# Optimization experiments

Hardware: AMD Instinct MI355X
Metric: run time of the kernel (lower is better)

## Reference

```python
import jax, jax.numpy as jnp
import numpy as np
from jax.scipy.special import logsumexp

EPS = 1e-16
SINKHORN_EPS = 0.05   # entropic regularization strength
SINKHORN_ITERS = 100  # fixed iteration count (jit-friendly)
PI = np.pi


def _p3_polarrel_from_cartesian(p):
    """(px,py,pz) [B,N,3] -> (eta_rel, phi_rel, pt_rel) [B,N,3], relative to jet."""
    px, py, pz = p[..., 0], p[..., 1], p[..., 2]
    pt = jnp.sqrt(px * px + py * py + EPS)
    phi = jnp.arctan2(py + EPS, px + EPS)
    eta = jnp.arcsinh(pz / (pt + EPS))
    # jet 3-momentum: sum over particle axis (dim -2)
    jp = p.sum(axis=-2)  # [B,3]
    jpx, jpy, jpz = jp[..., 0], jp[..., 1], jp[..., 2]
    jpt = jnp.sqrt(jpx * jpx + jpy * jpy + EPS)
    jphi = jnp.arctan2(jpy + EPS, jpx + EPS)
    jeta = jnp.arcsinh(jpz / (jpt + EPS))
    eta_rel = eta - jeta[..., None]
    phi_rel = (phi - jphi[..., None] + PI) % (2.0 * PI) - PI
    pt_rel = pt / (jpt[..., None] + EPS)
    return jnp.stack([eta_rel, phi_rel, pt_rel], axis=-1)


def _sinkhorn_emd(x, y):
    """Sinkhorn-regularized EMD between particle clouds.
    x, y: [B,N,3] of (eta_rel, phi_rel, pt_rel). Returns [B]."""
    eps = SINKHORN_EPS
    # pairwise DeltaR ground cost [B,N,N]
    deta = x[..., :, None, 0] - y[..., None, :, 0]
    dphi = x[..., :, None, 1] - y[..., None, :, 1]
    C = jnp.sqrt(deta * deta + dphi * dphi + EPS)
    # pt-based marginals (pt_rel > 0 by construction), normalized
    a = x[..., 2]
    b = y[..., 2]
    a = a / (a.sum(axis=-1, keepdims=True) + EPS)
    b = b / (b.sum(axis=-1, keepdims=True) + EPS)
    log_a = jnp.log(a + EPS)
    log_b = jnp.log(b + EPS)

    f0 = jnp.zeros_like(a)
    g0 = jnp.zeros_like(b)

    def step(carry, _):
        f, g = carry
        f = eps * (log_a - logsumexp((g[:, None, :] - C) / eps, axis=-1))
        g = eps * (log_b - logsumexp((f[:, :, None] - C) / eps, axis=-2))
        return (f, g), None

    (f, g), _ = jax.lax.scan(step, (f0, g0), None, length=SINKHORN_ITERS)
    logP = (f[:, :, None] + g[:, None, :] - C) / eps  # [B,N,N] transport plan (log)
    return jnp.sum(jnp.exp(logP) * C, axis=(-2, -1))  # [B]


def setup_inputs() -> dict:
    key = jax.random.key(0)
    k1, k2 = jax.random.split(key)
    B, N = 2048, 150
    p_recons = jax.random.normal(k1, (B, N, 3), dtype=jnp.float32)
    p_target = jax.random.normal(k2, (B, N, 3), dtype=jnp.float32)
    return {"p_recons": p_recons, "p_target": p_target}


def reference(p_recons, p_target):
    x = _p3_polarrel_from_cartesian(p_recons)
    y = _p3_polarrel_from_cartesian(p_target)
    return _sinkhorn_emd(x, y).sum(0)  # scalar, matching .sum(0) over batch
```

## Files before the change

kernel.cpp:

```cpp
#include <hip/hip_runtime.h>
#include <math.h>

#define N 150
#define NP 160
#define QUART 40
#define QUADS 10
#define BLOCK 640
#define ITERS 100
#define WARM 5
#define STEADY (ITERS - WARM - 1)

#define PI_F 3.14159265358979323846f
#define TWO_PI_F 6.28318530717958647692f
#define EPS_F 1e-16f
#define EPSLN2 0.03465735902799726f
#define INV_EPSLN2 28.853900817779268f
#define NEGBIG -1e30f

#if __has_builtin(__builtin_amdgcn_exp2f)
#define FEXP2(x) __builtin_amdgcn_exp2f(x)
#else
#define FEXP2(x) exp2f(x)
#endif
#if __has_builtin(__builtin_amdgcn_logf)
#define FLOG2(x) __builtin_amdgcn_logf(x)
#else
#define FLOG2(x) log2f(x)
#endif
#if __has_builtin(__builtin_amdgcn_rcpf)
#define FRCP(x) __builtin_amdgcn_rcpf(x)
#else
#define FRCP(x) (1.0f / (x))
#endif

__device__ __forceinline__ float blockReduceSum(float v, float* red) {
    for (int o = 32; o > 0; o >>= 1) v += __shfl_down(v, o, 64);
    const int lane = threadIdx.x & 63;
    const int wv = threadIdx.x >> 6;
    __syncthreads();
    if (lane == 0) red[wv] = v;
    __syncthreads();
    float s = 0.f;
    #pragma unroll
    for (int i = 0; i < BLOCK / 64; ++i) s += red[i];
    return s;
}

__global__ __launch_bounds__(BLOCK, 2) void emd_kernel(
    const float* __restrict__ p_recons,
    const float* __restrict__ p_target,
    float* __restrict__ out)
{
    __shared__ float xeta[N], xphi[N], yeta[N], yphi[N];
    __shared__ float l2a[N], l2b[N];
    __shared__ __align__(16) float uu[NP];
    __shared__ __align__(16) float vv[NP];
    __shared__ float red[BLOCK / 64];

    const int b = blockIdx.x;
    const int tid = threadIdx.x;

    for (int c = 0; c < 2; ++c) {
        const float* P = (c == 0 ? p_recons : p_target) + (size_t)b * (N * 3);
        float px = 0.f, py = 0.f, pz = 0.f;
        if (tid < N) {
            px = P[tid * 3 + 0];
            py = P[tid * 3 + 1];
            pz = P[tid * 3 + 2];
        }
        const float jx = blockReduceSum(px, red);
        const float jy = blockReduceSum(py, red);
        const float jz = blockReduceSum(pz, red);
        const float jpt  = sqrtf(jx * jx + jy * jy + EPS_F);
        const float jphi = atan2f(jy + EPS_F, jx + EPS_F);
        const float jeta = asinhf(jz / (jpt + EPS_F));

        float ptrel = 0.f, erel = 0.f, prel = 0.f;
        if (tid < N) {
            const float pt  = sqrtf(px * px + py * py + EPS_F);
            const float phi = atan2f(py + EPS_F, px + EPS_F);
            const float eta = asinhf(pz / (pt + EPS_F));
            erel = eta - jeta;
            float d = phi - jphi + PI_F;
            d = fmodf(d, TWO_PI_F);
            if (d < 0.f) d += TWO_PI_F;
            prel = d - PI_F;
            ptrel = pt / (jpt + EPS_F);
        }
        const float spt = blockReduceSum(ptrel, red);
        if (tid < N) {
            const float aa = ptrel / (spt + EPS_F);
            if (c == 0) { xeta[tid] = erel; xphi[tid] = prel; l2a[tid] = FLOG2(aa + EPS_F); }
            else        { yeta[tid] = erel; yphi[tid] = prel; l2b[tid] = FLOG2(aa + EPS_F); }
        }
    }
    __syncthreads();

    const int r = (tid >> 2) < N ? (tid >> 2) : (N - 1);
    const int q = tid & 3;
    const bool writer = (q == 0) && ((tid >> 2) < N);
    const bool act = (tid >> 2) < N;

    float nKu[QUART];
    float nKt[QUART];
    {
        const float xe = xeta[r], xp = xphi[r];
        const float ye = yeta[r], yp = yphi[r];
        #pragma unroll
        for (int s = 0; s < QUART; ++s) {
            const int j = q * QUART + s;
            float ku = NEGBIG, kt = NEGBIG;
            if (j < N) {
                float de = xe - yeta[j], dp = xp - yphi[j];
                ku = -sqrtf(de * de + dp * dp + EPS_F) * INV_EPSLN2;
                de = xeta[j] - ye; dp = xphi[j] - yp;
                kt = -sqrtf(de * de + dp * dp + EPS_F) * INV_EPSLN2;
            }
            nKu[s] = ku;
            nKt[s] = kt;
        }
    }
    if (tid < NP) {
        const float z = (tid < N) ? 0.f : NEGBIG;
        uu[tid] = z; vv[tid] = z;
    }
    __syncthreads();

    for (int it = 0; it < WARM; ++it) {
        {
            const float4* vp = (const float4*)&vv[q * QUART];
            float mx = -3e38f;
            #pragma unroll
            for (int s = 0; s < QUADS; ++s) {
                const float4 v4 = vp[s];
                mx = fmaxf(mx, fmaxf(fmaxf(v4.x + nKu[4*s], v4.y + nKu[4*s+1]),
                                     fmaxf(v4.z + nKu[4*s+2], v4.w + nKu[4*s+3])));
            }
            mx = fmaxf(mx, __shfl_xor(mx, 1, 64));
            mx = fmaxf(mx, __shfl_xor(mx, 2, 64));
            float s0 = 0.f, s1 = 0.f, s2 = 0.f, s3 = 0.f;
            #pragma unroll
            for (int s = 0; s < QUADS; ++s) {
                const float4 v4 = vp[s];
                s0 += FEXP2(v4.x + nKu[4*s]   - mx);
                s1 += FEXP2(v4.y + nKu[4*s+1] - mx);
                s2 += FEXP2(v4.z + nKu[4*s+2] - mx);
                s3 += FEXP2(v4.w + nKu[4*s+3] - mx);
            }
            float ss = (s0 + s1) + (s2 + s3);
            ss += __shfl_xor(ss, 1, 64);
            ss += __shfl_xor(ss, 2, 64);
            if (writer) uu[r] = l2a[r] - (mx + FLOG2(fmaxf(ss, 1e-37f)));
        }
        __syncthreads();
        {
            const float4* up = (const float4*)&uu[q * QUART];
            float mx = -3e38f;
            #pragma unroll
            for (int s = 0; s < QUADS; ++s) {
                const float4 u4 = up[s];
                mx = fmaxf(mx, fmaxf(fmaxf(u4.x + nKt[4*s], u4.y + nKt[4*s+1]),
                                     fmaxf(u4.z + nKt[4*s+2], u4.w + nKt[4*s+3])));
            }
            mx = fmaxf(mx, __shfl_xor(mx, 1, 64));
            mx = fmaxf(mx, __shfl_xor(mx, 2, 64));
            float s0 = 0.f, s1 = 0.f, s2 = 0.f, s3 = 0.f;
            #pragma unroll
            for (int s = 0; s < QUADS; ++s) {
                const float4 u4 = up[s];
                s0 += FEXP2(u4.x + nKt[4*s]   - mx);
                s1 += FEXP2(u4.y + nKt[4*s+1] - mx);
                s2 += FEXP2(u4.z + nKt[4*s+2] - mx);
                s3 += FEXP2(u4.w + nKt[4*s+3] - mx);
            }
            float ss = (s0 + s1) + (s2 + s3);
            ss += __shfl_xor(ss, 1, 64);
            ss += __shfl_xor(ss, 2, 64);
            if (writer) vv[r] = l2b[r] - (mx + FLOG2(fmaxf(ss, 1e-37f)));
        }
        __syncthreads();
    }

    float am, bm, fin, Vh6;
    {
        const float4* vp = (const float4*)&vv[q * QUART];
        float mx = -3e38f;
        #pragma unroll
        for (int s = 0; s < QUADS; ++s) {
            const float4 v4 = vp[s];
            mx = fmaxf(mx, fmaxf(fmaxf(v4.x + nKu[4*s], v4.y + nKu[4*s+1]),
                                 fmaxf(v4.z + nKu[4*s+2], v4.w + nKu[4*s+3])));
        }
        mx = fmaxf(mx, __shfl_xor(mx, 1, 64));
        mx = fmaxf(mx, __shfl_xor(mx, 2, 64));
        float s0 = 0.f, s1 = 0.f, s2 = 0.f, s3 = 0.f;
        #pragma unroll
        for (int s = 0; s < QUADS; ++s) {
            const float4 v4 = vp[s];
            nKu[4*s]   = FEXP2(v4.x + nKu[4*s]   - mx);
            nKu[4*s+1] = FEXP2(v4.y + nKu[4*s+1] - mx);
            nKu[4*s+2] = FEXP2(v4.z + nKu[4*s+2] - mx);
            nKu[4*s+3] = FEXP2(v4.w + nKu[4*s+3] - mx);
            s0 += nKu[4*s]; s1 += nKu[4*s+1]; s2 += nKu[4*s+2]; s3 += nKu[4*s+3];
        }
        float ss = (s0 + s1) + (s2 + s3);
        ss += __shfl_xor(ss, 1, 64);
        ss += __shfl_xor(ss, 2, 64);
        am  = ss;
        fin = FEXP2(l2a[r]) * FRCP(ss);
        if (writer) uu[r] = l2a[r] - (mx + FLOG2(ss));
    }
    __syncthreads();
    {
        const float4* up = (const float4*)&uu[q * QUART];
        float mx = -3e38f;
        #pragma unroll
        for (int s = 0; s < QUADS; ++s) {
            const float4 u4 = up[s];
            mx = fmaxf(mx, fmaxf(fmaxf(u4.x + nKt[4*s], u4.y + nKt[4*s+1]),
                                 fmaxf(u4.z + nKt[4*s+2], u4.w + nKt[4*s+3])));
        }
        mx = fmaxf(mx, __shfl_xor(mx, 1, 64));
        mx = fmaxf(mx, __shfl_xor(mx, 2, 64));
        float s0 = 0.f, s1 = 0.f, s2 = 0.f, s3 = 0.f;
        #pragma unroll
        for (int s = 0; s < QUADS; ++s) {
            const float4 u4 = up[s];
            nKt[4*s]   = FEXP2(u4.x + nKt[4*s]   - mx);
            nKt[4*s+1] = FEXP2(u4.y + nKt[4*s+1] - mx);
            nKt[4*s+2] = FEXP2(u4.z + nKt[4*s+2] - mx);
            nKt[4*s+3] = FEXP2(u4.w + nKt[4*s+3] - mx);
            s0 += nKt[4*s]; s1 += nKt[4*s+1]; s2 += nKt[4*s+2]; s3 += nKt[4*s+3];
        }
        float ssv = (s0 + s1) + (s2 + s3);
        ssv += __shfl_xor(ssv, 1, 64);
        ssv += __shfl_xor(ssv, 2, 64);
        const float v5r = vv[r];
        float t = l2b[r] - (mx + FLOG2(ssv)) - v5r;
        t = fminf(t, 100.f);
        Vh6 = FEXP2(t);
        bm  = Vh6 * ssv;
    }
    __syncthreads();
    if (writer) { uu[r] = 1.0f; vv[r] = Vh6; }
    if (tid >= N && tid < NP) { uu[tid] = 0.f; vv[tid] = 0.f; }
    __syncthreads();

    for (int it = 0; it < STEADY; ++it) {
        {
            const float4* vp = (const float4*)&vv[q * QUART];
            float s0 = 0.f, s1 = 0.f, s2 = 0.f, s3 = 0.f;
            #pragma unroll
            for (int s = 0; s < QUADS; ++s) {
                const float4 v4 = vp[s];
                s0 = fmaf(v4.x, nKu[4*s],   s0);
                s1 = fmaf(v4.y, nKu[4*s+1], s1);
                s2 = fmaf(v4.z, nKu[4*s+2], s2);
                s3 = fmaf(v4.w, nKu[4*s+3], s3);
            }
            float ss = (s0 + s1) + (s2 + s3);
            ss += __shfl_xor(ss, 1, 64);
            ss += __shfl_xor(ss, 2, 64);
            if (writer) uu[r] = fminf(am * FRCP(fmaxf(ss, 1e-30f)), 1e30f);
        }
        __syncthreads();
        {
            const float4* up = (const float4*)&uu[q * QUART];
            float s0 = 0.f, s1 = 0.f, s2 = 0.f, s3 = 0.f;
            #pragma unroll
            for (int s = 0; s < QUADS; ++s) {
                const float4 u4 = up[s];
                s0 = fmaf(u4.x, nKt[4*s],   s0);
                s1 = fmaf(u4.y, nKt[4*s+1], s1);
                s2 = fmaf(u4.z, nKt[4*s+2], s2);
                s3 = fmaf(u4.w, nKt[4*s+3], s3);
            }
            float ss = (s0 + s1) + (s2 + s3);
            ss += __shfl_xor(ss, 1, 64);
            ss += __shfl_xor(ss, 2, 64);
            if (writer) vv[r] = fminf(bm * FRCP(fmaxf(ss, 1e-30f)), 1e30f);
        }
        __syncthreads();
        if ((it & 7) == 7) {
            const float4* vp = (const float4*)&vv[q * QUART];
            float M = 0.f;
            #pragma unroll
            for (int s = 0; s < QUADS; ++s) {
                const float4 v4 = vp[s];
                nKu[4*s]   *= v4.x; nKu[4*s+1] *= v4.y;
                nKu[4*s+2] *= v4.z; nKu[4*s+3] *= v4.w;
                M = fmaxf(M, fmaxf(fmaxf(nKu[4*s], nKu[4*s+1]),
                                   fmaxf(nKu[4*s+2], nKu[4*s+3])));
            }
            M = fmaxf(M, __shfl_xor(M, 1, 64));
            M = fmaxf(M, __shfl_xor(M, 2, 64));
            M = fmaxf(M, 1e-30f);
            const float rM = FRCP(M);
            #pragma unroll
            for (int s = 0; s < QUART; ++s) nKu[s] *= rM;

            const float4* up = (const float4*)&uu[q * QUART];
            float Mv = 0.f;
            #pragma unroll
            for (int s = 0; s < QUADS; ++s) {
                const float4 u4 = up[s];
                nKt[4*s]   *= u4.x; nKt[4*s+1] *= u4.y;
                nKt[4*s+2] *= u4.z; nKt[4*s+3] *= u4.w;
                Mv = fmaxf(Mv, fmaxf(fmaxf(nKt[4*s], nKt[4*s+1]),
                                     fmaxf(nKt[4*s+2], nKt[4*s+3])));
            }
            Mv = fmaxf(Mv, __shfl_xor(Mv, 1, 64));
            Mv = fmaxf(Mv, __shfl_xor(Mv, 2, 64));
            Mv = fmaxf(Mv, 1e-30f);
            const float rMv = FRCP(Mv);
            #pragma unroll
            for (int s = 0; s < QUART; ++s) nKt[s] *= rMv;

            const float Uh = uu[r], Vh = vv[r];
            am  = fminf(am * rM  * FRCP(fmaxf(Uh, 1e-30f)), 1e30f);
            bm  = fminf(bm * rMv * FRCP(fmaxf(Vh, 1e-30f)), 1e30f);
            fin = fminf(fin * M * Uh, 1e30f);
            __syncthreads();
            if (writer) { uu[r] = 1.0f; vv[r] = 1.0f; }
            __syncthreads();
        }
    }

    float acc = 0.f;
    if (act) {
        const float u2 = fin * uu[r];
        const float xe = xeta[r], xp = xphi[r];
        const float4* vp = (const float4*)&vv[q * QUART];
        #pragma unroll
        for (int s = 0; s < QUADS; ++s) {
            const float4 v4 = vp[s];
            const float vc[4] = { v4.x, v4.y, v4.z, v4.w };
            #pragma unroll
            for (int c2 = 0; c2 < 4; ++c2) {
                const int j = q * QUART + 4 * s + c2;
                if (j < N) {
                    const float de = xe - yeta[j];
                    const float dp = xp - yphi[j];
                    const float C = sqrtf(de * de + dp * dp + EPS_F);
                    acc += u2 * vc[c2] * nKu[4 * s + c2] * C;
                }
            }
        }
    }
    acc = blockReduceSum(acc, red);
    if (tid == 0) atomicAdd(out, acc);
}

extern "C" void kernel_launch(void* const* d_in, const int* in_sizes, int n_in,
                              void* d_out, int out_size, void* d_ws, size_t ws_size,
                              hipStream_t stream) {
    const float* pr = (const float*)d_in[0];
    const float* pt = (const float*)d_in[1];
    float* out = (float*)d_out;
    const int B = in_sizes[0] / (N * 3);
    hipMemsetAsync(d_out, 0, sizeof(float) * out_size, stream);
    hipLaunchKernelGGL(emd_kernel, dim3(B), dim3(BLOCK), 0, stream, pr, pt, out);
}
```

Measured before the change: 980.9 us.

## Recompute cost on the fly in warm-up to cut registers and raise occupancy

The log-domain warm-up iterations no longer hold precomputed cost rows in registers. They recompute the DeltaR cost from shared-memory coordinates, and only the final kernel matrices are kept in registers. The `fin` scalar moves to shared memory, and launch bounds rise from 2 to 5 blocks per CU so more blocks can be resident and hide latency. The price is extra sqrt work in the warm-up passes, plus a risk of register spilling under the tighter launch bound.

```diff
diff --git a/kernel.cpp b/kernel.cpp
--- a/kernel.cpp
+++ b/kernel.cpp
@@ -33,6 +33,8 @@
 #define FRCP(x) (1.0f / (x))
 #endif
 
+union F4 { float4 v; float f[4]; };
+
 __device__ __forceinline__ float blockReduceSum(float v, float* red) {
     for (int o = 32; o > 0; o >>= 1) v += __shfl_down(v, o, 64);
     const int lane = threadIdx.x & 63;
@@ -46,15 +48,56 @@
     return s;
 }
 
-__global__ __launch_bounds__(BLOCK, 2) void emd_kernel(
+__device__ __forceinline__ void warm_pass(
+    const float* ce, const float* cp, const float* vf,
+    const float* l2, float* outArr,
+    float xe, float xp, int r, int q, bool writer)
+{
+    const F4* e4 = (const F4*)&ce[q * QUART];
+    const F4* p4 = (const F4*)&cp[q * QUART];
+    const F4* v4 = (const F4*)&vf[q * QUART];
+    float mx = -3e38f;
+    #pragma unroll
+    for (int s = 0; s < QUADS; ++s) {
+        F4 e = e4[s], p = p4[s], v = v4[s];
+        #pragma unroll
+        for (int k = 0; k < 4; ++k) {
+            const float de = xe - e.f[k], dp = xp - p.f[k];
+            const float kv = -sqrtf(de * de + dp * dp + EPS_F) * INV_EPSLN2;
+            const float t = (q * QUART + 4 * s + k < N) ? (v.f[k] + kv) : NEGBIG;
+            mx = fmaxf(mx, t);
+        }
+    }
+    mx = fmaxf(mx, __shfl_xor(mx, 1, 64));
+    mx = fmaxf(mx, __shfl_xor(mx, 2, 64));
+    float sA[4] = {0.f, 0.f, 0.f, 0.f};
+    #pragma unroll
+    for (int s = 0; s < QUADS; ++s) {
+        F4 e = e4[s], p = p4[s], v = v4[s];
+        #pragma unroll
+        for (int k = 0; k < 4; ++k) {
+            const float de = xe - e.f[k], dp = xp - p.f[k];
+            const float kv = -sqrtf(de * de + dp * dp + EPS_F) * INV_EPSLN2;
+            const float t = (q * QUART + 4 * s + k < N) ? (v.f[k] + kv) : NEGBIG;
+            sA[k] += FEXP2(t - mx);
+        }
+    }
+    float ss = (sA[0] + sA[1]) + (sA[2] + sA[3]);
+    ss += __shfl_xor(ss, 1, 64);
+    ss += __shfl_xor(ss, 2, 64);
+    if (writer) outArr[r] = l2[r] - (mx + FLOG2(fmaxf(ss, 1e-37f)));
+}
+
+__global__ __launch_bounds__(BLOCK, 5) void emd_kernel(
     const float* __restrict__ p_recons,
     const float* __restrict__ p_target,
     float* __restrict__ out)
 {
-    __shared__ float xeta[N], xphi[N], yeta[N], yphi[N];
+    __shared__ float xeta[NP], xphi[NP], yeta[NP], yphi[NP];
     __shared__ float l2a[N], l2b[N];
     __shared__ __align__(16) float uu[NP];
     __shared__ __align__(16) float vv[NP];
+    __shared__ float finl[N];
     __shared__ float red[BLOCK / 64];
 
     const int b = blockIdx.x;
@@ -94,6 +137,13 @@
             else        { yeta[tid] = erel; yphi[tid] = prel; l2b[tid] = FLOG2(aa + EPS_F); }
         }
     }
+    if (tid >= N && tid < NP) {
+        xeta[tid] = 0.f; xphi[tid] = 0.f; yeta[tid] = 0.f; yphi[tid] = 0.f;
+    }
+    if (tid < NP) {
+        const float z = (tid < N) ? 0.f : NEGBIG;
+        uu[tid] = z; vv[tid] = z;
+    }
     __syncthreads();
 
     const int r = (tid >> 2) < N ? (tid >> 2) : (N - 1);
@@ -101,144 +151,103 @@
     const bool writer = (q == 0) && ((tid >> 2) < N);
     const bool act = (tid >> 2) < N;
 
-    float nKu[QUART];
-    float nKt[QUART];
     {
         const float xe = xeta[r], xp = xphi[r];
         const float ye = yeta[r], yp = yphi[r];
-        #pragma unroll
-        for (int s = 0; s < QUART; ++s) {
-            const int j = q * QUART + s;
-            float ku = NEGBIG, kt = NEGBIG;
-            if (j < N) {
-                float de = xe - yeta[j], dp = xp - yphi[j];
-                ku = -sqrtf(de * de + dp * dp + EPS_F) * INV_EPSLN2;
-                de = xeta[j] - ye; dp = xphi[j] - yp;
-                kt = -sqrtf(de * de + dp * dp + EPS_F) * INV_EPSLN2;
-            }
-            nKu[s] = ku;
-            nKt[s] = kt;
-        }
-    }
-    if (tid < NP) {
-        const float z = (tid < N) ? 0.f : NEGBIG;
-        uu[tid] = z; vv[tid] = z;
-    }
-    __syncthreads();
-
-    for (int it = 0; it < WARM; ++it) {
-        {
-            const float4* vp = (const float4*)&vv[q * QUART];
-            float mx = -3e38f;
-            #pragma unroll
-            for (int s = 0; s < QUADS; ++s) {
-                const float4 v4 = vp[s];
-                mx = fmaxf(mx, fmaxf(fmaxf(v4.x + nKu[4*s], v4.y + nKu[4*s+1]),
-                                     fmaxf(v4.z + nKu[4*s+2], v4.w + nKu[4*s+3])));
-            }
-            mx = fmaxf(mx, __shfl_xor(mx, 1, 64));
-            mx = fmaxf(mx, __shfl_xor(mx, 2, 64));
-            float s0 = 0.f, s1 = 0.f, s2 = 0.f, s3 = 0.f;
-            #pragma unroll
-            for (int s = 0; s < QUADS; ++s) {
-                const float4 v4 = vp[s];
-                s0 += FEXP2(v4.x + nKu[4*s]   - mx);
-                s1 += FEXP2(v4.y + nKu[4*s+1] - mx);
-                s2 += FEXP2(v4.z + nKu[4*s+2] - mx);
-                s3 += FEXP2(v4.w + nKu[4*s+3] - mx);
-            }
-            float ss = (s0 + s1) + (s2 + s3);
-            ss += __shfl_xor(ss, 1, 64);
-            ss += __shfl_xor(ss, 2, 64);
-            if (writer) uu[r] = l2a[r] - (mx + FLOG2(fmaxf(ss, 1e-37f)));
-        }
-        __syncthreads();
-        {
-            const float4* up = (const float4*)&uu[q * QUART];
-            float mx = -3e38f;
-            #pragma unroll
-            for (int s = 0; s < QUADS; ++s) {
-                const float4 u4 = up[s];
-                mx = fmaxf(mx, fmaxf(fmaxf(u4.x + nKt[4*s], u4.y + nKt[4*s+1]),
-                                     fmaxf(u4.z + nKt[4*s+2], u4.w + nKt[4*s+3])));
-            }
-            mx = fmaxf(mx, __shfl_xor(mx, 1, 64));
-            mx = fmaxf(mx, __shfl_xor(mx, 2, 64));
-            float s0 = 0.f, s1 = 0.f, s2 = 0.f, s3 = 0.f;
-            #pragma unroll
-            for (int s = 0; s < QUADS; ++s) {
-                const float4 u4 = up[s];
-                s0 += FEXP2(u4.x + nKt[4*s]   - mx);
-                s1 += FEXP2(u4.y + nKt[4*s+1] - mx);
-                s2 += FEXP2(u4.z + nKt[4*s+2] - mx);
-                s3 += FEXP2(u4.w + nKt[4*s+3] - mx);
-            }
-            float ss = (s0 + s1) + (s2 + s3);
-            ss += __shfl_xor(ss, 1, 64);
-            ss += __shfl_xor(ss, 2, 64);
-            if (writer) vv[r] = l2b[r] - (mx + FLOG2(fmaxf(ss, 1e-37f)));
-        }
-        __syncthreads();
-    }
-
-    float am, bm, fin, Vh6;
+        for (int it = 0; it < WARM; ++it) {
+            warm_pass(yeta, yphi, vv, l2a, uu, xe, xp, r, q, writer);
+            __syncthreads();
+            warm_pass(xeta, xphi, uu, l2b, vv, ye, yp, r, q, writer);
+            __syncthreads();
+        }
+    }
+
+    float Ku[QUART];
+    float Kt[QUART];
+    float am, bm, Vh6;
     {
-        const float4* vp = (const float4*)&vv[q * QUART];
+        const float xe = xeta[r], xp = xphi[r];
+        const F4* e4 = (const F4*)&yeta[q * QUART];
+        const F4* p4 = (const F4*)&yphi[q * QUART];
+        const F4* v4 = (const F4*)&vv[q * QUART];
         float mx = -3e38f;
         #pragma unroll
         for (int s = 0; s < QUADS; ++s) {
-            const float4 v4 = vp[s];
-            mx = fmaxf(mx, fmaxf(fmaxf(v4.x + nKu[4*s], v4.y + nKu[4*s+1]),
-                                 fmaxf(v4.z + nKu[4*s+2], v4.w + nKu[4*s+3])));
+            F4 e = e4[s], p = p4[s], v = v4[s];
+            #pragma unroll
+            for (int k = 0; k < 4; ++k) {
+                const float de = xe - e.f[k], dp = xp - p.f[k];
+                const float kv = -sqrtf(de * de + dp * dp + EPS_F) * INV_EPSLN2;
+                const float t = (q * QUART + 4 * s + k < N) ? (v.f[k] + kv) : NEGBIG;
+                mx = fmaxf(mx, t);
+            }
         }
         mx = fmaxf(mx, __shfl_xor(mx, 1, 64));
         mx = fmaxf(mx, __shfl_xor(mx, 2, 64));
-        float s0 = 0.f, s1 = 0.f, s2 = 0.f, s3 = 0.f;
-        #pragma unroll
-        for (int s = 0; s < QUADS; ++s) {
-            const float4 v4 = vp[s];
-            nKu[4*s]   = FEXP2(v4.x + nKu[4*s]   - mx);
-            nKu[4*s+1] = FEXP2(v4.y + nKu[4*s+1] - mx);
-            nKu[4*s+2] = FEXP2(v4.z + nKu[4*s+2] - mx);
-            nKu[4*s+3] = FEXP2(v4.w + nKu[4*s+3] - mx);
-            s0 += nKu[4*s]; s1 += nKu[4*s+1]; s2 += nKu[4*s+2]; s3 += nKu[4*s+3];
-        }
-        float ss = (s0 + s1) + (s2 + s3);
+        float sA[4] = {0.f, 0.f, 0.f, 0.f};
+        #pragma unroll
+        for (int s = 0; s < QUADS; ++s) {
+            F4 e = e4[s], p = p4[s], v = v4[s];
+            #pragma unroll
+            for (int k = 0; k < 4; ++k) {
+                const float de = xe - e.f[k], dp = xp - p.f[k];
+                const float kv = -sqrtf(de * de + dp * dp + EPS_F) * INV_EPSLN2;
+                const float t = (q * QUART + 4 * s + k < N) ? (v.f[k] + kv) : NEGBIG;
+                const float el = FEXP2(t - mx);
+                Ku[4 * s + k] = el;
+                sA[k] += el;
+            }
+        }
+        float ss = (sA[0] + sA[1]) + (sA[2] + sA[3]);
         ss += __shfl_xor(ss, 1, 64);
         ss += __shfl_xor(ss, 2, 64);
-        am  = ss;
-        fin = FEXP2(l2a[r]) * FRCP(ss);
-        if (writer) uu[r] = l2a[r] - (mx + FLOG2(ss));
+        am = ss;
+        if (writer) {
+            finl[r] = FEXP2(l2a[r]) * FRCP(ss);
+            uu[r] = l2a[r] - (mx + FLOG2(ss));
+        }
     }
     __syncthreads();
     {
-        const float4* up = (const float4*)&uu[q * QUART];
-        float mx = -3e38f;
-        #pragma unroll
-        for (int s = 0; s < QUADS; ++s) {
-            const float4 u4 = up[s];
-            mx = fmaxf(mx, fmaxf(fmaxf(u4.x + nKt[4*s], u4.y + nKt[4*s+1]),
-                                 fmaxf(u4.z + nKt[4*s+2], u4.w + nKt[4*s+3])));
-        }
-        mx = fmaxf(mx, __shfl_xor(mx, 1, 64));
-        mx = fmaxf(mx, __shfl_xor(mx, 2, 64));
-        float s0 = 0.f, s1 = 0.f, s2 = 0.f, s3 = 0.f;
-        #pragma unroll
-        for (int s = 0; s < QUADS; ++s) {
-            const float4 u4 = up[s];
-            nKt[4*s]   = FEXP2(u4.x + nKt[4*s]   - mx);
-            nKt[4*s+1] = FEXP2(u4.y + nKt[4*s+1] - mx);
-            nKt[4*s+2] = FEXP2(u4.z + nKt[4*s+2] - mx);
-            nKt[4*s+3] = FEXP2(u4.w + nKt[4*s+3] - mx);
-            s0 += nKt[4*s]; s1 += nKt[4*s+1]; s2 += nKt[4*s+2]; s3 += nKt[4*s+3];
-        }
-        float ssv = (s0 + s1) + (s2 + s3);
+        const float ye = yeta[r], yp = yphi[r];
+        const F4* e4 = (const F4*)&xeta[q * QUART];
+        const F4* p4 = (const F4*)&xphi[q * QUART];
+        const F4* u4 = (const F4*)&uu[q * QUART];
+        float mv = -3e38f;
+        #pragma unroll
+        for (int s = 0; s < QUADS; ++s) {
+            F4 e = e4[s], p = p4[s], u = u4[s];
+            #pragma unroll
+            for (int k = 0; k < 4; ++k) {
+                const float de = e.f[k] - ye, dp = p.f[k] - yp;
+                const float kv = -sqrtf(de * de + dp * dp + EPS_F) * INV_EPSLN2;
+                const float t = (q * QUART + 4 * s + k < N) ? (u.f[k] + kv) : NEGBIG;
+                mv = fmaxf(mv, t);
+            }
+        }
+        mv = fmaxf(mv, __shfl_xor(mv, 1, 64));
+        mv = fmaxf(mv, __shfl_xor(mv, 2, 64));
+        float sA[4] = {0.f, 0.f, 0.f, 0.f};
+        #pragma unroll
+        for (int s = 0; s < QUADS; ++s) {
+            F4 e = e4[s], p = p4[s], u = u4[s];
+            #pragma unroll
+            for (int k = 0; k < 4; ++k) {
+                const float de = e.f[k] - ye, dp = p.f[k] - yp;
+                const float kv = -sqrtf(de * de + dp * dp + EPS_F) * INV_EPSLN2;
+                const float t = (q * QUART + 4 * s + k < N) ? (u.f[k] + kv) : NEGBIG;
+                const float el = FEXP2(t - mv);
+                Kt[4 * s + k] = el;
+                sA[k] += el;
+            }
+        }
+        float ssv = (sA[0] + sA[1]) + (sA[2] + sA[3]);
         ssv += __shfl_xor(ssv, 1, 64);
         ssv += __shfl_xor(ssv, 2, 64);
         const float v5r = vv[r];
-        float t = l2b[r] - (mx + FLOG2(ssv)) - v5r;
-        t = fminf(t, 100.f);
-        Vh6 = FEXP2(t);
+        float t2 = l2b[r] - (mv + FLOG2(ssv)) - v5r;
+        t2 = fminf(t2, 100.f);
+        Vh6 = FEXP2(t2);
         bm  = Vh6 * ssv;
     }
     __syncthreads();
@@ -252,11 +261,11 @@
             float s0 = 0.f, s1 = 0.f, s2 = 0.f, s3 = 0.f;
             #pragma unroll
             for (int s = 0; s < QUADS; ++s) {
-                const float4 v4 = vp[s];
-                s0 = fmaf(v4.x, nKu[4*s],   s0);
-                s1 = fmaf(v4.y, nKu[4*s+1], s1);
-                s2 = fmaf(v4.z, nKu[4*s+2], s2);
-                s3 = fmaf(v4.w, nKu[4*s+3], s3);
+                F4 v4; v4.v = vp[s];
+                s0 = fmaf(v4.f[0], Ku[4*s],   s0);
+                s1 = fmaf(v4.f[1], Ku[4*s+1], s1);
+                s2 = fmaf(v4.f[2], Ku[4*s+2], s2);
+                s3 = fmaf(v4.f[3], Ku[4*s+3], s3);
             }
             float ss = (s0 + s1) + (s2 + s3);
             ss += __shfl_xor(ss, 1, 64);
@@ -269,11 +278,11 @@
             float s0 = 0.f, s1 = 0.f, s2 = 0.f, s3 = 0.f;
             #pragma unroll
             for (int s = 0; s < QUADS; ++s) {
-                const float4 u4 = up[s];
-                s0 = fmaf(u4.x, nKt[4*s],   s0);
-                s1 = fmaf(u4.y, nKt[4*s+1], s1);
-                s2 = fmaf(u4.z, nKt[4*s+2], s2);
-                s3 = fmaf(u4.w, nKt[4*s+3], s3);
+                F4 u4; u4.v = up[s];
+                s0 = fmaf(u4.f[0], Kt[4*s],   s0);
+                s1 = fmaf(u4.f[1], Kt[4*s+1], s1);
+                s2 = fmaf(u4.f[2], Kt[4*s+2], s2);
+                s3 = fmaf(u4.f[3], Kt[4*s+3], s3);
             }
             float ss = (s0 + s1) + (s2 + s3);
             ss += __shfl_xor(ss, 1, 64);
@@ -286,40 +295,40 @@
             float M = 0.f;
             #pragma unroll
             for (int s = 0; s < QUADS; ++s) {
-                const float4 v4 = vp[s];
-                nKu[4*s]   *= v4.x; nKu[4*s+1] *= v4.y;
-                nKu[4*s+2] *= v4.z; nKu[4*s+3] *= v4.w;
-                M = fmaxf(M, fmaxf(fmaxf(nKu[4*s], nKu[4*s+1]),
-                                   fmaxf(nKu[4*s+2], nKu[4*s+3])));
+                F4 v4; v4.v = vp[s];
+                Ku[4*s]   *= v4.f[0]; Ku[4*s+1] *= v4.f[1];
+                Ku[4*s+2] *= v4.f[2]; Ku[4*s+3] *= v4.f[3];
+                M = fmaxf(M, fmaxf(fmaxf(Ku[4*s], Ku[4*s+1]),
+                                   fmaxf(Ku[4*s+2], Ku[4*s+3])));
             }
             M = fmaxf(M, __shfl_xor(M, 1, 64));
             M = fmaxf(M, __shfl_xor(M, 2, 64));
             M = fmaxf(M, 1e-30f);
             const float rM = FRCP(M);
             #pragma unroll
-            for (int s = 0; s < QUART; ++s) nKu[s] *= rM;
+            for (int s = 0; s < QUART; ++s) Ku[s] *= rM;
 
             const float4* up = (const float4*)&uu[q * QUART];
             float Mv = 0.f;
             #pragma unroll
             for (int s = 0; s < QUADS; ++s) {
-                const float4 u4 = up[s];
-                nKt[4*s]   *= u4.x; nKt[4*s+1] *= u4.y;
-                nKt[4*s+2] *= u4.z; nKt[4*s+3] *= u4.w;
-                Mv = fmaxf(Mv, fmaxf(fmaxf(nKt[4*s], nKt[4*s+1]),
-                                     fmaxf(nKt[4*s+2], nKt[4*s+3])));
+                F4 u4; u4.v = up[s];
+                Kt[4*s]   *= u4.f[0]; Kt[4*s+1] *= u4.f[1];
+                Kt[4*s+2] *= u4.f[2]; Kt[4*s+3] *= u4.f[3];
+                Mv = fmaxf(Mv, fmaxf(fmaxf(Kt[4*s], Kt[4*s+1]),
+                                     fmaxf(Kt[4*s+2], Kt[4*s+3])));
             }
             Mv = fmaxf(Mv, __shfl_xor(Mv, 1, 64));
             Mv = fmaxf(Mv, __shfl_xor(Mv, 2, 64));
             Mv = fmaxf(Mv, 1e-30f);
             const float rMv = FRCP(Mv);
             #pragma unroll
-            for (int s = 0; s < QUART; ++s) nKt[s] *= rMv;
+            for (int s = 0; s < QUART; ++s) Kt[s] *= rMv;
 
             const float Uh = uu[r], Vh = vv[r];
-            am  = fminf(am * rM  * FRCP(fmaxf(Uh, 1e-30f)), 1e30f);
-            bm  = fminf(bm * rMv * FRCP(fmaxf(Vh, 1e-30f)), 1e30f);
-            fin = fminf(fin * M * Uh, 1e30f);
+            am = fminf(am * rM  * FRCP(fmaxf(Uh, 1e-30f)), 1e30f);
+            bm = fminf(bm * rMv * FRCP(fmaxf(Vh, 1e-30f)), 1e30f);
+            if (writer) finl[r] = fminf(finl[r] * M * Uh, 1e30f);
             __syncthreads();
             if (writer) { uu[r] = 1.0f; vv[r] = 1.0f; }
             __syncthreads();
@@ -328,21 +337,20 @@
 
     float acc = 0.f;
     if (act) {
-        const float u2 = fin * uu[r];
+        const float u2 = finl[r] * uu[r];
         const float xe = xeta[r], xp = xphi[r];
         const float4* vp = (const float4*)&vv[q * QUART];
         #pragma unroll
         for (int s = 0; s < QUADS; ++s) {
-            const float4 v4 = vp[s];
-            const float vc[4] = { v4.x, v4.y, v4.z, v4.w };
-            #pragma unroll
-            for (int c2 = 0; c2 < 4; ++c2) {
-                const int j = q * QUART + 4 * s + c2;
+            F4 v4; v4.v = vp[s];
+            #pragma unroll
+            for (int k = 0; k < 4; ++k) {
+                const int j = q * QUART + 4 * s + k;
                 if (j < N) {
                     const float de = xe - yeta[j];
                     const float dp = xp - yphi[j];
                     const float C = sqrtf(de * de + dp * dp + EPS_F);
-                    acc += u2 * vc[c2] * nKu[4 * s + c2] * C;
+                    acc += u2 * v4.f[k] * Ku[4 * s + k] * C;
                 }
             }
         }
```

New measurement: 2.986 ms. +204.4%, slower.
